# Kernel tuning notes

Measured on AMD Instinct MI355X. Metric: run time of the kernel, lower is better.

The kernel has to match this reference:

```python
import jax, jax.numpy as jnp
import numpy as np

H = 8  # number_heads

def setup_inputs() -> dict:
    key = jax.random.key(0)
    ks = jax.random.split(key, 10)
    B, Nx, Ny, Qd, Kd, Vd = 4, 2048, 2048, 512, 512, 512
    s = 0.02
    return {
        "X": jax.random.normal(ks[0], (B, Nx, Qd), jnp.float32),
        "Y": jax.random.normal(ks[1], (B, Ny, Kd), jnp.float32),
        "Wq": jax.random.normal(ks[2], (Vd, Qd), jnp.float32) * s,
        "bq": jax.random.normal(ks[3], (Vd,), jnp.float32) * s,
        "Wk": jax.random.normal(ks[4], (Vd, Kd), jnp.float32) * s,
        "bk": jax.random.normal(ks[5], (Vd,), jnp.float32) * s,
        "Wv": jax.random.normal(ks[6], (Vd, Kd), jnp.float32) * s,
        "bv": jax.random.normal(ks[7], (Vd,), jnp.float32) * s,
        "Wo": jax.random.normal(ks[8], (Vd, Vd), jnp.float32) * s,
        "bo": jax.random.normal(ks[9], (Vd,), jnp.float32) * s,
    }

def reference(X, Y, Wq, bq, Wk, bk, Wv, bv, Wo, bo):
    B, Nq, _ = X.shape
    Nk = Y.shape[1]
    Vd = Wq.shape[0]
    d = Vd // H  # head dim (dim_split)
    # QKV projections (torch Linear: x @ W^T + b)
    Q = (X @ Wq.T + bq).reshape(B, Nq, H, d)
    K = (Y @ Wk.T + bk).reshape(B, Nk, H, d)
    V = (Y @ Wv.T + bv).reshape(B, Nk, H, d)
    # attention: softmax(Q K^T / sqrt(d)) per head
    scores = jnp.einsum("bqhd,bkhd->bhqk", Q, K) / jnp.sqrt(jnp.float32(d))
    attn = jax.nn.softmax(scores, axis=-1)
    # residual on Q (pre-output-proj), per the original: O = Q_split + Attn @ V_split
    O = Q + jnp.einsum("bhqk,bkhd->bqhd", attn, V)
    O = O.reshape(B, Nq, Vd)  # concat heads back
    return O @ Wo.T + bo
```

## Files before the change

kernel.cpp:

```cpp
#include <hip/hip_runtime.h>
#include <hip/hip_bf16.h>

typedef unsigned short u16;
typedef __attribute__((ext_vector_type(4))) float f32x4;
typedef __attribute__((ext_vector_type(16))) float f32x16;
typedef __attribute__((ext_vector_type(8))) short bf16x8;
typedef __attribute__((ext_vector_type(4))) int i32x4;
typedef __attribute__((ext_vector_type(4))) unsigned short u16x4;

#define DEVI static __device__ __forceinline__

DEVI u16 f2bf(float f) {
  __hip_bfloat16 h = __float2bfloat16(f);
  return *reinterpret_cast<u16*>(&h);
}
DEVI float bf2f(u16 u) {
  unsigned int x = ((unsigned int)u) << 16;
  return __uint_as_float(x);
}
DEVI float exp2a(float x) {
  float r;
  asm("v_exp_f32 %0, %1" : "=v"(r) : "v"(x));
  return r;
}
DEVI int cvtpk(float lo, float hi) {
  int r;
  asm("v_cvt_pk_bf16_f32 %0, %1, %2" : "=v"(r) : "v"(lo), "v"(hi));
  return r;
}
DEVI f32x16 mfma32(bf16x8 a, bf16x8 b, f32x16 c) {
  return __builtin_amdgcn_mfma_f32_32x32x16_bf16(a, b, c, 0, 0, 0);
}
DEVI float xhalf_sum(float x) {
  float a = x, b;
  asm volatile("v_mov_b32 %0, %1" : "=v"(b) : "v"(x));
  asm volatile("v_permlane32_swap_b32 %0, %1" : "+v"(a), "+v"(b));
  return a + b;
}

DEVI void gload_lds16(const void* g, void* l) {
  __builtin_amdgcn_global_load_lds(
      (const __attribute__((address_space(1))) unsigned int*)g,
      (__attribute__((address_space(3))) unsigned int*)l, 16, 0, 0);
}

#define BAR() __builtin_amdgcn_s_barrier()
#define WAITV0() asm volatile("s_waitcnt vmcnt(0)" ::: "memory")
#define WAITV1() asm volatile("s_waitcnt vmcnt(1)" ::: "memory")

__global__ __launch_bounds__(256) void k_convall(
    const float* __restrict__ X, const float* __restrict__ Y,
    const float* __restrict__ Wq, const float* __restrict__ Wk,
    const float* __restrict__ Wv, const float* __restrict__ Wo,
    u16* __restrict__ Xb, u16* __restrict__ Yb, u16* __restrict__ Wb) {
  long i = ((long)blockIdx.x * 256 + threadIdx.x) * 8;
  const float* s;
  u16* d;
  long off;
  if (i < 4194304) {
    s = X; d = Xb; off = i;
  } else if (i < 8388608) {
    s = Y; d = Yb; off = i - 4194304;
  } else {
    long w = (i - 8388608) >> 18;
    off = (i - 8388608) & 262143;
    s = w == 0 ? Wq : w == 1 ? Wk : w == 2 ? Wv : Wo;
    d = Wb + w * 262144;
  }
  f32x4 a = *(const f32x4*)(s + off);
  f32x4 b = *(const f32x4*)(s + off + 4);
  bf16x8 v;
#pragma unroll
  for (int j = 0; j < 4; ++j) {
    v[j]     = (short)f2bf(a[j]);
    v[4 + j] = (short)f2bf(b[j]);
  }
  *(bf16x8*)(d + off) = v;
}

struct GemmAcc { f32x4 acc[4][2]; };

DEVI void gemm_body(const u16* __restrict__ A, const u16* __restrict__ Bw,
                    int m0, int n0, char* sm, GemmAcc& G) {
  const int tid = threadIdx.x;
  const int wid = tid >> 6, lane = tid & 63;
  const int g = lane >> 4, li = lane & 15;
  const int wr = wid >> 1, wc = wid & 1;

  int arow[4], acol[4];
#pragma unroll
  for (int i = 0; i < 4; ++i) {
    int P0 = ((i * 4 + wid) << 10) + lane * 16;
    int L0 = P0 ^ (((P0 >> 7) & 7) << 4);
    arow[i] = L0 >> 7;
    acol[i] = L0 & 127;
  }

#pragma unroll
  for (int mr = 0; mr < 4; ++mr)
#pragma unroll
    for (int nr = 0; nr < 2; ++nr) G.acc[mr][nr] = (f32x4){0.f, 0.f, 0.f, 0.f};

  auto stage = [&](int kt, int half) {
    char* As = sm + half * 24576;
    char* Bs = As + 16384;
    const int k0b = kt * 128;
#pragma unroll
    for (int i = 0; i < 4; ++i)
      gload_lds16((const char*)A + (size_t)(m0 + arow[i]) * 1024 + k0b + acol[i],
                  As + ((i * 4 + wid) << 10));
#pragma unroll
    for (int i = 0; i < 2; ++i)
      gload_lds16((const char*)Bw + (size_t)(n0 + arow[i]) * 1024 + k0b + acol[i],
                  Bs + ((i * 4 + wid) << 10));
  };

  stage(0, 0);
#pragma unroll 1
  for (int kt = 0; kt < 8; ++kt) {
    const int half = kt & 1;
    if (kt < 7) {
      stage(kt + 1, half ^ 1);
      asm volatile("s_waitcnt vmcnt(6)" ::: "memory");
    } else {
      asm volatile("s_waitcnt vmcnt(0)" ::: "memory");
    }
    BAR();
    const char* As = sm + half * 24576;
    const char* Bs = As + 16384;
#pragma unroll
    for (int ks = 0; ks < 2; ++ks) {
      bf16x8 af[4], bfr[2];
#pragma unroll
      for (int mr = 0; mr < 4; ++mr) {
        int row = wr * 64 + mr * 16 + li;
        int L = row * 128 + ks * 64 + g * 16;
        int P = L ^ ((row & 7) << 4);
        af[mr] = *(const bf16x8*)(As + P);
      }
#pragma unroll
      for (int nr = 0; nr < 2; ++nr) {
        int row = wc * 32 + nr * 16 + li;
        int L = row * 128 + ks * 64 + g * 16;
        int P = L ^ ((row & 7) << 4);
        bfr[nr] = *(const bf16x8*)(Bs + P);
      }
#pragma unroll
      for (int mr = 0; mr < 4; ++mr)
#pragma unroll
        for (int nr = 0; nr < 2; ++nr)
          G.acc[mr][nr] = __builtin_amdgcn_mfma_f32_16x16x32_bf16(
              af[mr], bfr[nr], G.acc[mr][nr], 0, 0, 0);
    }
    BAR();
  }
}

__global__ __launch_bounds__(256) void k_gemm_qkv(
    const u16* __restrict__ Xb, const u16* __restrict__ Yb,
    const u16* __restrict__ Wall, const float* __restrict__ bq,
    const float* __restrict__ bk, const float* __restrict__ bv,
    u16* __restrict__ Qb, u16* __restrict__ Kb, u16* __restrict__ Vtb) {
  __shared__ __align__(16) char sm[49152];
  const int z = blockIdx.z;
  int lin = blockIdx.x + 8 * blockIdx.y;
  int xcd = lin & 7, slot = lin >> 3;

  const u16 *Ag, *Bg;
  int m0, n0;
  if (z == 2) {
    Ag = Wall + 2 * 262144;
    Bg = Yb;
    m0 = (slot >> 4) * 128;
    n0 = (xcd * 16 + (slot & 15)) * 64;
  } else {
    Ag = z ? Yb : Xb;
    Bg = Wall + (size_t)z * 262144;
    m0 = (xcd * 8 + (slot >> 3)) * 128;
    n0 = (slot & 7) * 64;
  }

  GemmAcc G;
  gemm_body(Ag, Bg, m0, n0, sm, G);

  const int tid = threadIdx.x;
  const int wid = tid >> 6, lane = tid & 63;
  const int g = lane >> 4, li = lane & 15;
  const int wr = wid >> 1, wc = wid & 1;

  if (z <= 1) {
    u16* Cout = z ? Kb : Qb;
    const float* bias = z ? bk : bq;
#pragma unroll
    for (int nr = 0; nr < 2; ++nr) {
      int col = n0 + wc * 32 + nr * 16 + li;
      float bvv = bias[col];
#pragma unroll
      for (int mr = 0; mr < 4; ++mr) {
#pragma unroll
        for (int j = 0; j < 4; ++j) {
          int row = m0 + wr * 64 + mr * 16 + g * 4 + j;
          float v = G.acc[mr][nr][j] + bvv;
          int b = row >> 11, nn = row & 2047, h = col >> 6, dd = col & 63;
          Cout[(((size_t)(b * 8 + h) << 11) + nn) * 64 + dd] = f2bf(v);
        }
      }
    }
  } else {
#pragma unroll
    for (int mr = 0; mr < 4; ++mr) {
#pragma unroll
      for (int j = 0; j < 4; ++j) {
        int row = m0 + wr * 64 + mr * 16 + g * 4 + j;
        float bvv = bv[row];
        int hh = row >> 6, dd = row & 63;
#pragma unroll
        for (int nr = 0; nr < 2; ++nr) {
          int col = n0 + wc * 32 + nr * 16 + li;
          int b = col >> 11, nn = col & 2047;
          Vtb[(((size_t)(b * 8 + hh) * 64) + dd) * 2048 + nn] =
              f2bf(G.acc[mr][nr][j] + bvv);
        }
      }
    }
  }
}

__global__ __launch_bounds__(256) void k_gemm_out(const u16* __restrict__ A,
                                                  const u16* __restrict__ Bw,
                                                  const float* __restrict__ bias,
                                                  float* __restrict__ Cout) {
  __shared__ __align__(16) char sm[49152];
  int lin = blockIdx.x + 8 * blockIdx.y;
  int xcd = lin & 7, slot = lin >> 3;
  int by = xcd * 8 + (slot >> 3), bx = slot & 7;
  const int m0 = by * 128, n0 = bx * 64;

  GemmAcc G;
  gemm_body(A, Bw, m0, n0, sm, G);

  const int tid = threadIdx.x;
  const int wid = tid >> 6, lane = tid & 63;
  const int g = lane >> 4, li = lane & 15;
  const int wr = wid >> 1, wc = wid & 1;
#pragma unroll
  for (int nr = 0; nr < 2; ++nr) {
    int col = n0 + wc * 32 + nr * 16 + li;
    float bvv = bias[col];
#pragma unroll
    for (int mr = 0; mr < 4; ++mr) {
#pragma unroll
      for (int j = 0; j < 4; ++j) {
        int row = m0 + wr * 64 + mr * 16 + g * 4 + j;
        Cout[(size_t)row * 512 + col] = G.acc[mr][nr][j] + bvv;
      }
    }
  }
}

DEVI void qk32(const char* L, int KB, const int* vK, const bf16x8* qf, f32x16& r) {
  const f32x16 Z = {};
  bf16x8 kf;
  kf = *(const bf16x8*)(L + (vK[0] + KB)); r = mfma32(kf, qf[0], Z);
  kf = *(const bf16x8*)(L + (vK[1] + KB)); r = mfma32(kf, qf[1], r);
  kf = *(const bf16x8*)(L + (vK[2] + KB)); r = mfma32(kf, qf[2], r);
  kf = *(const bf16x8*)(L + (vK[3] + KB)); r = mfma32(kf, qf[3], r);
}

DEVI void sm_pv32(const char* L, int VB, const int* vV, f32x16& s,
                  f32x16& o0, f32x16& o1, float& lsum) {
#pragma unroll
  for (int i = 0; i < 16; ++i) s[i] = exp2a(s[i]);
  float t4[4];
#pragma unroll
  for (int i = 0; i < 4; ++i)
    t4[i] = (s[4 * i] + s[4 * i + 1]) + (s[4 * i + 2] + s[4 * i + 3]);
  lsum += (t4[0] + t4[1]) + (t4[2] + t4[3]);

#pragma unroll
  for (int kt = 0; kt < 2; ++kt) {
    const int base = kt * 8;
    int a0 = cvtpk(s[base + 0], s[base + 1]);
    int a1 = cvtpk(s[base + 2], s[base + 3]);
    int b0 = cvtpk(s[base + 4], s[base + 5]);
    int b1 = cvtpk(s[base + 6], s[base + 7]);
    asm volatile("v_permlane32_swap_b32 %0, %1" : "+v"(a0), "+v"(b0));
    asm volatile("v_permlane32_swap_b32 %0, %1" : "+v"(a1), "+v"(b1));
    i32x4 pi = {a0, a1, b0, b1};
    bf16x8 pb = __builtin_bit_cast(bf16x8, pi);
    bf16x8 va = *(const bf16x8*)(L + (vV[kt] + VB));
    o0 = mfma32(va, pb, o0);
    va = *(const bf16x8*)(L + (vV[kt] + VB + 2048));
    o1 = mfma32(va, pb, o1);
  }
}

__global__ __launch_bounds__(512, 4) void k_attn(const u16* __restrict__ Qb,
                                                 const u16* __restrict__ Kb,
                                                 const u16* __restrict__ Vt,
                                                 u16* __restrict__ Ob) {
  __shared__ __align__(16) char lds[33792];
  const int tid = threadIdx.x, wid = tid >> 6, lane = tid & 63;
  const int li = lane & 31, h = lane >> 5;
  const int grp = wid >> 2, w4 = wid & 3;

  const int lin = blockIdx.x;
  const int xcd = lin & 7, slot = lin >> 3;
  const int bh = xcd * 4 + (slot >> 4);
  const int qt = slot & 15;
  const int start = (slot * 3) & 31;

  const u16* Qh = Qb + ((size_t)bh << 11) * 64;
  const u16* Kh = Kb + ((size_t)bh << 11) * 64;
  const u16* Vh = Vt + (size_t)bh * 64 * 2048;

  int vK[4], vV[2];
  {
    const int swzK = (li & 7) << 4;
#pragma unroll
    for (int k4 = 0; k4 < 4; ++k4) vK[k4] = li * 128 + ((k4 * 32 + h * 16) ^ swzK);
    const int swzV = (li & 3) << 4;
#pragma unroll
    for (int kt = 0; kt < 2; ++kt) vV[kt] = li * 64 + ((kt * 32 + h * 16) ^ swzV);
  }

  const int q = qt * 128 + w4 * 32 + li;
  const float C2 = 0.18033688f;
  bf16x8 qf[4];
#pragma unroll
  for (int k4 = 0; k4 < 4; ++k4) {
    bf16x8 f = *(const bf16x8*)(Qh + (size_t)q * 64 + k4 * 16 + h * 8);
    bf16x8 r;
#pragma unroll
    for (int e = 0; e < 4; ++e) {
      int p = cvtpk(bf2f((u16)f[2 * e]) * C2, bf2f((u16)f[2 * e + 1]) * C2);
      r[2 * e]     = (short)(p & 0xffff);
      r[2 * e + 1] = (short)((unsigned)p >> 16);
    }
    qf[k4] = r;
  }

  const int PK = (w4 << 10) + (lane << 4);
  const int LK = PK ^ (((PK >> 7) & 7) << 4);
  const int LV = PK ^ (((PK >> 6) & 3) << 4);
  const int vgo = (LV >> 6) * 4096 + (LV & 63);

  char* gb = lds + grp * 16384;
  const char* Lg = gb;

  auto T = [&](int n) { return grp * 32 + ((start + n) & 31); };
  auto stageK = [&](int tt, int kb) {
    gload_lds16((const char*)Kh + (size_t)tt * 4096 + LK, gb + kb + (w4 << 10));
  };
  auto stageV = [&](int tt, int vb) {
    gload_lds16((const char*)Vh + (size_t)tt * 64 + vgo, gb + vb + (w4 << 10));
  };

  f32x16 o0 = {}, o1 = {};
  f32x16 sA, sB;
  float lsum = 0.f;

  stageK(T(0), 0);
  stageV(T(0), 8192);
  stageK(T(1), 4096);
  stageV(T(1), 12288);
  WAITV0();
  BAR();
  qk32(Lg, 0, vK, qf, sA);

#pragma unroll 1
  for (int it = 0; it < 15; ++it) {
    const int t = it * 2;
    WAITV1();
    BAR();
    stageK(T(t + 2), 0);
    qk32(Lg, 4096, vK, qf, sB);
    sm_pv32(Lg, 8192, vV, sA, o0, o1, lsum);
    BAR();
    stageV(T(t + 2), 8192);
    WAITV1();
    BAR();
    stageK(T(t + 3), 4096);
    qk32(Lg, 0, vK, qf, sA);
    sm_pv32(Lg, 12288, vV, sB, o0, o1, lsum);
    BAR();
    stageV(T(t + 3), 12288);
  }
  WAITV1();
  BAR();
  qk32(Lg, 4096, vK, qf, sB);
  sm_pv32(Lg, 8192, vV, sA, o0, o1, lsum);
  WAITV0();
  BAR();
  sm_pv32(Lg, 12288, vV, sB, o0, o1, lsum);

  __syncthreads();
  if (grp == 1) {
#pragma unroll
    for (int j = 0; j < 8; ++j) {
      const f32x16& o = (j < 4) ? o0 : o1;
      const int s2 = (j & 3) * 4;
      f32x4 c = {o[s2 + 0], o[s2 + 1], o[s2 + 2], o[s2 + 3]};
      *(f32x4*)(lds + w4 * 8192 + j * 1024 + lane * 16) = c;
    }
    ((float*)(lds + 32768))[w4 * 64 + lane] = lsum;
  }
  __syncthreads();
  if (grp == 0) {
#pragma unroll
    for (int j = 0; j < 8; ++j) {
      f32x4 c = *(const f32x4*)(lds + w4 * 8192 + j * 1024 + lane * 16);
      f32x16& o = (j < 4) ? o0 : o1;
      const int s2 = (j & 3) * 4;
      o[s2 + 0] += c[0]; o[s2 + 1] += c[1]; o[s2 + 2] += c[2]; o[s2 + 3] += c[3];
    }
    lsum += ((const float*)(lds + 32768))[w4 * 64 + lane];
    const float inv = 1.0f / xhalf_sum(lsum);

    const int b = bh >> 3, head = bh & 7;
    u16* orow = Ob + ((size_t)(b * 2048 + q)) * 512 + head * 64;
    const u16* qrow = Qh + (size_t)q * 64;
#pragma unroll
    for (int dt = 0; dt < 2; ++dt) {
      const f32x16& o = dt ? o1 : o0;
#pragma unroll
      for (int s2 = 0; s2 < 4; ++s2) {
        int d0 = dt * 32 + s2 * 8 + h * 4;
        u16x4 qv = *(const u16x4*)(qrow + d0);
        u16x4 w;
#pragma unroll
        for (int j = 0; j < 4; ++j)
          w[j] = f2bf(fmaf(o[s2 * 4 + j], inv, bf2f(qv[j])));
        *(u16x4*)(orow + d0) = w;
      }
    }
  }
}

extern "C" void kernel_launch(void* const* d_in, const int* in_sizes, int n_in,
                              void* d_out, int out_size, void* d_ws, size_t ws_size,
                              hipStream_t stream) {
  const float* X  = (const float*)d_in[0];
  const float* Y  = (const float*)d_in[1];
  const float* Wq = (const float*)d_in[2];
  const float* bq = (const float*)d_in[3];
  const float* Wk = (const float*)d_in[4];
  const float* bk = (const float*)d_in[5];
  const float* Wv = (const float*)d_in[6];
  const float* bv = (const float*)d_in[7];
  const float* Wo = (const float*)d_in[8];
  const float* bo = (const float*)d_in[9];

  char* ws = (char*)d_ws;
  u16* Xb  = (u16*)(ws);
  u16* Yb  = (u16*)(ws + (size_t)(8  << 20));
  u16* Wb  = (u16*)(ws + (size_t)(16 << 20));
  u16* Qb  = (u16*)(ws + (size_t)(18 << 20));
  u16* Kb  = (u16*)(ws + (size_t)(26 << 20));
  u16* Vtb = (u16*)(ws + (size_t)(34 << 20));
  u16* Ob  = (u16*)(ws + (size_t)(42 << 20));

  k_convall<<<4608, 256, 0, stream>>>(X, Y, Wq, Wk, Wv, Wo, Xb, Yb, Wb);

  k_gemm_qkv<<<dim3(8, 64, 3), 256, 0, stream>>>(Xb, Yb, Wb, bq, bk, bv, Qb, Kb, Vtb);

  k_attn<<<512, 512, 0, stream>>>(Qb, Kb, Vtb, Ob);

  k_gemm_out<<<dim3(8, 64), 256, 0, stream>>>(Ob, Wb + 3 * 262144, bo, (float*)d_out);
}
```

Measured before the change: 88.30 us.

## Double the attention key tile to 64 and simplify the double-buffered pipeline

The attention kernel now processes 64 keys per tile instead of 32. K and V for a tile are staged together into one buffer, and the loop becomes a plain double-buffered loop with one compute step and two barriers per tile, in place of interleaved QK and softmax-PV stages. The aim is to cut barriers and waits per key, and to batch more MFMA and exp work between syncs. In exchange, LDS per block roughly doubles to 64KB, which can reduce the number of resident blocks under launch_bounds(512,4). The QK of the next tile no longer overlaps with the PV of the current one inside a wave.

```diff
diff --git a/kernel.cpp b/kernel.cpp
--- a/kernel.cpp
+++ b/kernel.cpp
@@ -46,7 +46,7 @@
 
 #define BAR() __builtin_amdgcn_s_barrier()
 #define WAITV0() asm volatile("s_waitcnt vmcnt(0)" ::: "memory")
-#define WAITV1() asm volatile("s_waitcnt vmcnt(1)" ::: "memory")
+#define WAITV4() asm volatile("s_waitcnt vmcnt(4)" ::: "memory")
 
 __global__ __launch_bounds__(256) void k_convall(
     const float* __restrict__ X, const float* __restrict__ Y,
@@ -258,40 +258,51 @@
   }
 }
 
-DEVI void qk32(const char* L, int KB, const int* vK, const bf16x8* qf, f32x16& r) {
+DEVI void attn_tile64(const char* L, int KB, const int* v4, const bf16x8* qf,
+                      f32x16& o0, f32x16& o1, float& lsum) {
+  const int VB = KB + 8192;
   const f32x16 Z = {};
+  f32x16 s0, s1;
   bf16x8 kf;
-  kf = *(const bf16x8*)(L + (vK[0] + KB)); r = mfma32(kf, qf[0], Z);
-  kf = *(const bf16x8*)(L + (vK[1] + KB)); r = mfma32(kf, qf[1], r);
-  kf = *(const bf16x8*)(L + (vK[2] + KB)); r = mfma32(kf, qf[2], r);
-  kf = *(const bf16x8*)(L + (vK[3] + KB)); r = mfma32(kf, qf[3], r);
-}
-
-DEVI void sm_pv32(const char* L, int VB, const int* vV, f32x16& s,
-                  f32x16& o0, f32x16& o1, float& lsum) {
-#pragma unroll
-  for (int i = 0; i < 16; ++i) s[i] = exp2a(s[i]);
-  float t4[4];
-#pragma unroll
-  for (int i = 0; i < 4; ++i)
-    t4[i] = (s[4 * i] + s[4 * i + 1]) + (s[4 * i + 2] + s[4 * i + 3]);
-  lsum += (t4[0] + t4[1]) + (t4[2] + t4[3]);
-
-#pragma unroll
-  for (int kt = 0; kt < 2; ++kt) {
-    const int base = kt * 8;
-    int a0 = cvtpk(s[base + 0], s[base + 1]);
-    int a1 = cvtpk(s[base + 2], s[base + 3]);
-    int b0 = cvtpk(s[base + 4], s[base + 5]);
-    int b1 = cvtpk(s[base + 6], s[base + 7]);
-    asm volatile("v_permlane32_swap_b32 %0, %1" : "+v"(a0), "+v"(b0));
-    asm volatile("v_permlane32_swap_b32 %0, %1" : "+v"(a1), "+v"(b1));
-    i32x4 pi = {a0, a1, b0, b1};
-    bf16x8 pb = __builtin_bit_cast(bf16x8, pi);
-    bf16x8 va = *(const bf16x8*)(L + (vV[kt] + VB));
-    o0 = mfma32(va, pb, o0);
-    va = *(const bf16x8*)(L + (vV[kt] + VB + 2048));
-    o1 = mfma32(va, pb, o1);
+  kf = *(const bf16x8*)(L + KB + v4[0]);        s0 = mfma32(kf, qf[0], Z);
+  kf = *(const bf16x8*)(L + KB + 4096 + v4[0]); s1 = mfma32(kf, qf[0], Z);
+  kf = *(const bf16x8*)(L + KB + v4[1]);        s0 = mfma32(kf, qf[1], s0);
+  kf = *(const bf16x8*)(L + KB + 4096 + v4[1]); s1 = mfma32(kf, qf[1], s1);
+  kf = *(const bf16x8*)(L + KB + v4[2]);        s0 = mfma32(kf, qf[2], s0);
+  kf = *(const bf16x8*)(L + KB + 4096 + v4[2]); s1 = mfma32(kf, qf[2], s1);
+  kf = *(const bf16x8*)(L + KB + v4[3]);        s0 = mfma32(kf, qf[3], s0);
+  kf = *(const bf16x8*)(L + KB + 4096 + v4[3]); s1 = mfma32(kf, qf[3], s1);
+
+#pragma unroll
+  for (int i = 0; i < 16; ++i) s0[i] = exp2a(s0[i]);
+#pragma unroll
+  for (int i = 0; i < 16; ++i) s1[i] = exp2a(s1[i]);
+  float t8[8];
+#pragma unroll
+  for (int i = 0; i < 8; ++i)
+    t8[i] = (s0[2 * i] + s0[2 * i + 1]) + (s1[2 * i] + s1[2 * i + 1]);
+  lsum += ((t8[0] + t8[1]) + (t8[2] + t8[3])) + ((t8[4] + t8[5]) + (t8[6] + t8[7]));
+
+#pragma unroll
+  for (int half = 0; half < 2; ++half) {
+    const f32x16& sp = half ? s1 : s0;
+#pragma unroll
+    for (int kt = 0; kt < 2; ++kt) {
+      const int base = kt * 8;
+      int a0 = cvtpk(sp[base + 0], sp[base + 1]);
+      int a1 = cvtpk(sp[base + 2], sp[base + 3]);
+      int b0 = cvtpk(sp[base + 4], sp[base + 5]);
+      int b1 = cvtpk(sp[base + 6], sp[base + 7]);
+      asm volatile("v_permlane32_swap_b32 %0, %1" : "+v"(a0), "+v"(b0));
+      asm volatile("v_permlane32_swap_b32 %0, %1" : "+v"(a1), "+v"(b1));
+      i32x4 pi = {a0, a1, b0, b1};
+      bf16x8 pb = __builtin_bit_cast(bf16x8, pi);
+      const int s = half * 2 + kt;
+      bf16x8 va = *(const bf16x8*)(L + VB + v4[s]);
+      o0 = mfma32(va, pb, o0);
+      va = *(const bf16x8*)(L + VB + 4096 + v4[s]);
+      o1 = mfma32(va, pb, o1);
+    }
   }
 }
 
@@ -299,7 +310,7 @@
                                                  const u16* __restrict__ Kb,
                                                  const u16* __restrict__ Vt,
                                                  u16* __restrict__ Ob) {
-  __shared__ __align__(16) char lds[33792];
+  __shared__ __align__(16) char lds[65536];
   const int tid = threadIdx.x, wid = tid >> 6, lane = tid & 63;
   const int li = lane & 31, h = lane >> 5;
   const int grp = wid >> 2, w4 = wid & 3;
@@ -308,20 +319,17 @@
   const int xcd = lin & 7, slot = lin >> 3;
   const int bh = xcd * 4 + (slot >> 4);
   const int qt = slot & 15;
-  const int start = (slot * 3) & 31;
+  const int start = (slot * 3) & 15;
 
   const u16* Qh = Qb + ((size_t)bh << 11) * 64;
   const u16* Kh = Kb + ((size_t)bh << 11) * 64;
   const u16* Vh = Vt + (size_t)bh * 64 * 2048;
 
-  int vK[4], vV[2];
+  int v4[4];
   {
-    const int swzK = (li & 7) << 4;
-#pragma unroll
-    for (int k4 = 0; k4 < 4; ++k4) vK[k4] = li * 128 + ((k4 * 32 + h * 16) ^ swzK);
-    const int swzV = (li & 3) << 4;
-#pragma unroll
-    for (int kt = 0; kt < 2; ++kt) vV[kt] = li * 64 + ((kt * 32 + h * 16) ^ swzV);
+    const int swz = (li & 7) << 4;
+#pragma unroll
+    for (int s = 0; s < 4; ++s) v4[s] = li * 128 + ((s * 32 + h * 16) ^ swz);
   }
 
   const int q = qt * 128 + w4 * 32 + li;
@@ -340,59 +348,50 @@
     qf[k4] = r;
   }
 
-  const int PK = (w4 << 10) + (lane << 4);
-  const int LK = PK ^ (((PK >> 7) & 7) << 4);
-  const int LV = PK ^ (((PK >> 6) & 3) << 4);
-  const int vgo = (LV >> 6) * 4096 + (LV & 63);
-
-  char* gb = lds + grp * 16384;
+  char* gb = lds + grp * 32768;
   const char* Lg = gb;
-
-  auto T = [&](int n) { return grp * 32 + ((start + n) & 31); };
-  auto stageK = [&](int tt, int kb) {
-    gload_lds16((const char*)Kh + (size_t)tt * 4096 + LK, gb + kb + (w4 << 10));
+  int ksrc[2], vsrc[2];
+#pragma unroll
+  for (int j = 0; j < 2; ++j) {
+    int P0 = w4 * 2048 + j * 1024 + lane * 16;
+    int L0 = P0 ^ (((P0 >> 7) & 7) << 4);
+    ksrc[j] = L0;
+    vsrc[j] = (L0 >> 7) * 4096 + (L0 & 127);
+  }
+
+  auto T = [&](int n) { return grp * 16 + ((start + n) & 15); };
+  auto stage = [&](int tt, int bb) {
+#pragma unroll
+    for (int j = 0; j < 2; ++j)
+      gload_lds16((const char*)Kh + (size_t)tt * 8192 + ksrc[j],
+                  gb + bb + w4 * 2048 + j * 1024);
+#pragma unroll
+    for (int j = 0; j < 2; ++j)
+      gload_lds16((const char*)Vh + (size_t)tt * 128 + vsrc[j],
+                  gb + bb + 8192 + w4 * 2048 + j * 1024);
   };
-  auto stageV = [&](int tt, int vb) {
-    gload_lds16((const char*)Vh + (size_t)tt * 64 + vgo, gb + vb + (w4 << 10));
-  };
 
   f32x16 o0 = {}, o1 = {};
-  f32x16 sA, sB;
   float lsum = 0.f;
 
-  stageK(T(0), 0);
-  stageV(T(0), 8192);
-  stageK(T(1), 4096);
-  stageV(T(1), 12288);
+  stage(T(0), 0);
+  stage(T(1), 16384);
+  WAITV4();
+  BAR();
+
+#pragma unroll 1
+  for (int it = 0; it < 14; ++it) {
+    const int cur = (it & 1) * 16384;
+    attn_tile64(Lg, cur, v4, qf, o0, o1, lsum);
+    BAR();
+    stage(T(it + 2), cur);
+    WAITV4();
+    BAR();
+  }
+  attn_tile64(Lg, 0, v4, qf, o0, o1, lsum);
   WAITV0();
   BAR();
-  qk32(Lg, 0, vK, qf, sA);
-
-#pragma unroll 1
-  for (int it = 0; it < 15; ++it) {
-    const int t = it * 2;
-    WAITV1();
-    BAR();
-    stageK(T(t + 2), 0);
-    qk32(Lg, 4096, vK, qf, sB);
-    sm_pv32(Lg, 8192, vV, sA, o0, o1, lsum);
-    BAR();
-    stageV(T(t + 2), 8192);
-    WAITV1();
-    BAR();
-    stageK(T(t + 3), 4096);
-    qk32(Lg, 0, vK, qf, sA);
-    sm_pv32(Lg, 12288, vV, sB, o0, o1, lsum);
-    BAR();
-    stageV(T(t + 3), 12288);
-  }
-  WAITV1();
-  BAR();
-  qk32(Lg, 4096, vK, qf, sB);
-  sm_pv32(Lg, 8192, vV, sA, o0, o1, lsum);
-  WAITV0();
-  BAR();
-  sm_pv32(Lg, 12288, vV, sB, o0, o1, lsum);
+  attn_tile64(Lg, 16384, v4, qf, o0, o1, lsum);
 
   __syncthreads();
   if (grp == 1) {
```

Result: no change. 86.80 us (-1.7%).
